# Kernel tuning notes

Measured on AMD Instinct MI355X. Metric: run time of the kernel, lower is better.

## Reference

```python
import jax, jax.numpy as jnp
import numpy as np

RADIUS = 0.4
NSAMPLE = 32
NORMALIZE_DP = True


def setup_inputs() -> dict:
    key = jax.random.key(0)
    k1, k2, k3 = jax.random.split(key, 3)
    B, N, K, C = 2, 16384, 4096, 128
    xyz = jax.random.normal(k1, (B, N, 3), dtype=jnp.float32)
    new_xyz = jax.random.normal(k2, (B, K, 3), dtype=jnp.float32)
    features = jax.random.normal(k3, (B, C, N), dtype=jnp.float32)
    return {"xyz": xyz, "new_xyz": new_xyz, "features": features}


def _ball_query(radius, nsample, xyz, new_xyz):
    # xyz: (B,N,3), new_xyz: (B,K,3) -> indices (B,K,nsample) int32
    N = xyz.shape[1]
    # squared distances via ||a||^2 + ||b||^2 - 2 a.b  -> (B,K,N)
    d2 = (jnp.sum(new_xyz * new_xyz, -1)[:, :, None]
          + jnp.sum(xyz * xyz, -1)[:, None, :]
          - 2.0 * jnp.einsum('bkd,bnd->bkn', new_xyz, xyz))
    mask = d2 < radius * radius
    # key = point index if inside ball else N (sentinel); take nsample smallest
    key = jnp.where(mask, jnp.arange(N, dtype=jnp.int32), jnp.int32(N))
    neg_top, _ = jax.lax.top_k(-key, nsample)  # (B,K,nsample)
    idx = -neg_top
    # pointnet2 semantics: pad with first in-radius index (0 if ball empty)
    first = idx[..., :1]
    first = jnp.where(first < N, first, 0)
    idx = jnp.where(idx < N, idx, first)
    return idx


def _group(features, idx):
    # features: (B,C,N), idx: (B,K,ns) -> (B,C,K,ns)
    return jax.vmap(lambda f, i: f[:, i])(features, idx)


def reference(xyz, new_xyz, features):
    idx = _ball_query(RADIUS, NSAMPLE, xyz, new_xyz)          # (B,K,ns)
    xyz_t = jnp.transpose(xyz, (0, 2, 1))                      # (B,3,N)
    grouped_xyz = _group(xyz_t, idx)                           # (B,3,K,ns)
    grouped_xyz = grouped_xyz - jnp.transpose(new_xyz, (0, 2, 1))[..., None]
    if NORMALIZE_DP:
        grouped_xyz = grouped_xyz / RADIUS
    grouped_features = _group(features, idx)                   # (B,C,K,ns)
    return (grouped_xyz, grouped_features)
```

## Files before the change

### kernel.cpp

```cpp
#include <hip/hip_runtime.h>

#define BB 2
#define NN 16384
#define KK 4096
#define CC 128
#define SS 32
#define BKK (BB * KK)

typedef float vfloat4 __attribute__((ext_vector_type(4)));

__global__ __launch_bounds__(1024) void prep_sort_kernel(
    const float* __restrict__ xyz, const float* __restrict__ new_xyz,
    float* __restrict__ xyzw, int* __restrict__ qmap)
{
    const int t = threadIdx.x;

    if (blockIdx.x == 0) {
        __shared__ int hist[64];
        __shared__ int base[64];
        __shared__ unsigned char bk[BKK];

        if (t < 64) hist[t] = 0;
        __syncthreads();

#pragma unroll
        for (int c = 0; c < BKK / 1024; ++c) {
            const int q = c * 1024 + t;
            const float* p = new_xyz + (size_t)q * 3;
            const float qq = p[0] * p[0] + p[1] * p[1] + p[2] * p[2];
            int bkt = (int)(qq * 8.0f);
            bkt = bkt > 63 ? 63 : bkt;
            bk[q] = (unsigned char)bkt;
            atomicAdd(&hist[bkt], 1);
        }
        __syncthreads();

        if (t == 0) {
            int s = 0;
#pragma unroll
            for (int i = 0; i < 64; ++i) { base[i] = s; s += hist[i]; }
        }
        __syncthreads();

#pragma unroll
        for (int c = 0; c < BKK / 1024; ++c) {
            const int q = c * 1024 + t;
            const int pos = atomicAdd(&base[bk[q]], 1);
            qmap[pos] = q;
        }
    } else {
        const int i = (blockIdx.x - 1) * 1024 + t;
        const float* p = xyz + (size_t)i * 3;
        const float x = p[0], y = p[1], z = p[2];
        const float pp = __fadd_rn(__fadd_rn(__fmul_rn(x, x), __fmul_rn(y, y)),
                                   __fmul_rn(z, z));
        vfloat4 v = {x, y, z, pp};
        *(vfloat4*)(xyzw + (size_t)i * 4) = v;
    }
}

__global__ __launch_bounds__(256) void ball_transpose_kernel(
    const float* __restrict__ xyzw,
    const float* __restrict__ new_xyz,
    const int* __restrict__ qmap,
    const float* __restrict__ feat,
    int* __restrict__ idx_buf,
    float* __restrict__ feat_t)
{
    __shared__ float tile[32][133];

    const int t = threadIdx.x;

    if (blockIdx.x < BKK / 4) {
        const int wave = t >> 6;
        const int lane = t & 63;
        const int qi   = qmap[blockIdx.x * 4 + wave];
        const int b    = qi >> 12;
        const int k    = qi & (KK - 1);

        const float R2 = (float)(0.4 * 0.4);

        const float* q = new_xyz + (size_t)(b * KK + k) * 3;
        const float qx = q[0], qy = q[1], qz = q[2];
        const float qq = __fadd_rn(__fadd_rn(__fmul_rn(qx, qx), __fmul_rn(qy, qy)),
                                   __fmul_rn(qz, qz));

        const vfloat4* xw = (const vfloat4*)xyzw + (size_t)b * NN;
        int* out = idx_buf + (size_t)qi * SS;

        int cnt = 0;
        int first = -1;

        auto process = [&](int base, vfloat4 v) {
            const float dot = __fadd_rn(__fadd_rn(__fmul_rn(qx, v.x), __fmul_rn(qy, v.y)),
                                        __fmul_rn(qz, v.z));
            const float d2 = __fsub_rn(__fadd_rn(qq, v.w), __fmul_rn(2.0f, dot));
            const bool inball = d2 < R2;
            const unsigned long long mask = __ballot(inball);
            if (mask) {
                if (first < 0) first = base + (int)__builtin_ctzll(mask);
                if (inball) {
                    const int pos = cnt + __popcll(mask & ((1ull << lane) - 1ull));
                    if (pos < SS) out[pos] = base + lane;
                }
                cnt += __popcll(mask);
            }
        };

        vfloat4 v0 = xw[lane];
        vfloat4 v1 = xw[64 + lane];
        vfloat4 v2 = xw[128 + lane];
        vfloat4 v3 = xw[192 + lane];

        for (int base = 0; base < NN; base += 256) {
            const int nb = (base + 256 < NN) ? base + 256 : 0;
            vfloat4 u0 = xw[nb + lane];
            vfloat4 u1 = xw[nb + 64 + lane];
            vfloat4 u2 = xw[nb + 128 + lane];
            vfloat4 u3 = xw[nb + 192 + lane];

            process(base, v0);
            process(base + 64, v1);
            process(base + 128, v2);
            process(base + 192, v3);
            if (cnt >= SS) break;

            v0 = u0; v1 = u1; v2 = u2; v3 = u3;
        }

        const int fill = (first < 0) ? 0 : first;
        if (lane < SS && lane >= cnt) out[lane] = fill;
    } else {
        const int tb = blockIdx.x - BKK / 4;
        const int b  = tb >> 9;
        const int n0 = (tb & 511) * 32;

#pragma unroll
        for (int i = 0; i < 4; ++i) {
            const int li = i * 256 + t;
            const int c  = li >> 3;
            const int n4 = (li & 7) * 4;
            const vfloat4 v = *(const vfloat4*)(feat + ((size_t)b * CC + c) * NN + n0 + n4);
            tile[n4 + 0][c] = v.x;
            tile[n4 + 1][c] = v.y;
            tile[n4 + 2][c] = v.z;
            tile[n4 + 3][c] = v.w;
        }
        __syncthreads();

#pragma unroll
        for (int i = 0; i < 4; ++i) {
            const int li = i * 256 + t;
            const int n  = li >> 5;
            const int c4 = (li & 31) * 4;
            vfloat4 v;
            v.x = tile[n][c4 + 0];
            v.y = tile[n][c4 + 1];
            v.z = tile[n][c4 + 2];
            v.w = tile[n][c4 + 3];
            *(vfloat4*)(feat_t + ((size_t)(b * NN + n0 + n)) * CC + c4) = v;
        }
    }
}

__global__ __launch_bounds__(256) void group_kernel(
    const float* __restrict__ xyzw,
    const float* __restrict__ new_xyz,
    const float* __restrict__ feat_t,
    const int*   __restrict__ idx_buf,
    float* __restrict__ out)
{
    __shared__ float tile[SS * CC];
    __shared__ float txyz[3][SS];

    const int t    = threadIdx.x;
    const int l    = t & 63;
    const int w    = t >> 6;
    const int bk   = blockIdx.x;
    const int b    = bk >> 12;
    const int k    = bk & (KK - 1);
    const int half = l >> 5;
    const int cl   = l & 31;

#pragma unroll
    for (int p = 0; p < 4; ++p) {
        const int r = 8 * w + 2 * p;
        const int s = r + half;
        const int n = idx_buf[bk * SS + s];
        const int chunk = cl ^ ((s >> 2) & 7);
        const float* src = feat_t + ((size_t)(b * NN + n)) * CC + 4 * chunk;
        __builtin_amdgcn_global_load_lds(
            (const __attribute__((address_space(1))) void*)src,
            (__attribute__((address_space(3))) void*)(tile + r * CC),
            16, 0, 0);
    }

    if (t < SS) {
        const int n = idx_buf[bk * SS + t];
        const float* q = new_xyz + (size_t)bk * 3;
        const vfloat4 wv = *((const vfloat4*)xyzw + (size_t)b * NN + n);
        txyz[0][t] = (wv.x - q[0]) / 0.4f;
        txyz[1][t] = (wv.y - q[1]) / 0.4f;
        txyz[2][t] = (wv.z - q[2]) / 0.4f;
    }

    __syncthreads();

    float* out_xyz  = out;
    float* out_feat = out + (size_t)BB * 3 * KK * SS;

    const int sq = t & 7;
    const int c0 = t >> 3;
#pragma unroll
    for (int p = 0; p < 4; ++p) {
        const int c  = c0 + 32 * p;
        const int co = (((c >> 2) ^ sq) << 2) + (c & 3);
        vfloat4 v;
        v.x = tile[(4 * sq + 0) * CC + co];
        v.y = tile[(4 * sq + 1) * CC + co];
        v.z = tile[(4 * sq + 2) * CC + co];
        v.w = tile[(4 * sq + 3) * CC + co];
        __builtin_nontemporal_store(
            v, (vfloat4*)(out_feat + (((size_t)(b * CC + c) * KK + k) * SS + 4 * sq)));
    }

    if (t < 24) {
        const int d   = t >> 3;
        const int sq2 = t & 7;
        const vfloat4 v = *(vfloat4*)&txyz[d][4 * sq2];
        __builtin_nontemporal_store(
            v, (vfloat4*)(out_xyz + (((size_t)(b * 3 + d) * KK + k) * SS + 4 * sq2)));
    }
}

extern "C" void kernel_launch(void* const* d_in, const int* in_sizes, int n_in,
                              void* d_out, int out_size, void* d_ws, size_t ws_size,
                              hipStream_t stream) {
    const float* xyz     = (const float*)d_in[0];
    const float* new_xyz = (const float*)d_in[1];
    const float* feat    = (const float*)d_in[2];
    float* out = (float*)d_out;

    int*   idx_buf = (int*)d_ws;
    float* xyzw    = (float*)((char*)d_ws + (1 << 20));
    float* feat_t  = (float*)((char*)d_ws + (1 << 20) + (512 << 10));
    int*   qmap    = (int*)((char*)d_ws + (1 << 20) + (512 << 10) + (CC * NN * BB) * 4);

    prep_sort_kernel<<<dim3(33), dim3(1024), 0, stream>>>(
        xyz, new_xyz, xyzw, qmap);

    ball_transpose_kernel<<<dim3(BKK / 4 + BB * (NN / 32)), dim3(256), 0, stream>>>(
        xyzw, new_xyz, qmap, feat, idx_buf, feat_t);

    group_kernel<<<dim3(BKK), dim3(256), 0, stream>>>(
        xyzw, new_xyz, feat_t, idx_buf, out);
}
```

Before: 82.67 us.

## Double-buffer two queries per group block and halve ball-query block size

```diff
diff --git a/kernel.cpp b/kernel.cpp
--- a/kernel.cpp
+++ b/kernel.cpp
@@ -59,7 +59,7 @@
     }
 }
 
-__global__ __launch_bounds__(256) void ball_transpose_kernel(
+__global__ __launch_bounds__(128) void ball_transpose_kernel(
     const float* __restrict__ xyzw,
     const float* __restrict__ new_xyz,
     const int* __restrict__ qmap,
@@ -71,10 +71,10 @@
 
     const int t = threadIdx.x;
 
-    if (blockIdx.x < BKK / 4) {
+    if (blockIdx.x < BKK / 2) {
         const int wave = t >> 6;
         const int lane = t & 63;
-        const int qi   = qmap[blockIdx.x * 4 + wave];
+        const int qi   = qmap[blockIdx.x * 2 + wave];
         const int b    = qi >> 12;
         const int k    = qi & (KK - 1);
 
@@ -131,13 +131,13 @@
         const int fill = (first < 0) ? 0 : first;
         if (lane < SS && lane >= cnt) out[lane] = fill;
     } else {
-        const int tb = blockIdx.x - BKK / 4;
+        const int tb = blockIdx.x - BKK / 2;
         const int b  = tb >> 9;
         const int n0 = (tb & 511) * 32;
 
 #pragma unroll
-        for (int i = 0; i < 4; ++i) {
-            const int li = i * 256 + t;
+        for (int i = 0; i < 8; ++i) {
+            const int li = i * 128 + t;
             const int c  = li >> 3;
             const int n4 = (li & 7) * 4;
             const vfloat4 v = *(const vfloat4*)(feat + ((size_t)b * CC + c) * NN + n0 + n4);
@@ -149,8 +149,8 @@
         __syncthreads();
 
 #pragma unroll
-        for (int i = 0; i < 4; ++i) {
-            const int li = i * 256 + t;
+        for (int i = 0; i < 8; ++i) {
+            const int li = i * 128 + t;
             const int n  = li >> 5;
             const int c4 = (li & 31) * 4;
             vfloat4 v;
@@ -170,66 +170,124 @@
     const int*   __restrict__ idx_buf,
     float* __restrict__ out)
 {
-    __shared__ float tile[SS * CC];
-    __shared__ float txyz[3][SS];
+    __shared__ float tileA[SS * CC];
+    __shared__ float tileB[SS * CC];
+    __shared__ float txyzA[3][SS];
+    __shared__ float txyzB[3][SS];
 
     const int t    = threadIdx.x;
     const int l    = t & 63;
     const int w    = t >> 6;
-    const int bk   = blockIdx.x;
-    const int b    = bk >> 12;
-    const int k    = bk & (KK - 1);
+    const int bk0  = blockIdx.x * 2;
+    const int bk1  = bk0 + 1;
     const int half = l >> 5;
     const int cl   = l & 31;
 
-#pragma unroll
-    for (int p = 0; p < 4; ++p) {
-        const int r = 8 * w + 2 * p;
-        const int s = r + half;
-        const int n = idx_buf[bk * SS + s];
-        const int chunk = cl ^ ((s >> 2) & 7);
-        const float* src = feat_t + ((size_t)(b * NN + n)) * CC + 4 * chunk;
-        __builtin_amdgcn_global_load_lds(
-            (const __attribute__((address_space(1))) void*)src,
-            (__attribute__((address_space(3))) void*)(tile + r * CC),
-            16, 0, 0);
-    }
-
-    if (t < SS) {
-        const int n = idx_buf[bk * SS + t];
-        const float* q = new_xyz + (size_t)bk * 3;
-        const vfloat4 wv = *((const vfloat4*)xyzw + (size_t)b * NN + n);
-        txyz[0][t] = (wv.x - q[0]) / 0.4f;
-        txyz[1][t] = (wv.y - q[1]) / 0.4f;
-        txyz[2][t] = (wv.z - q[2]) / 0.4f;
-    }
-
-    __syncthreads();
-
     float* out_xyz  = out;
     float* out_feat = out + (size_t)BB * 3 * KK * SS;
 
-    const int sq = t & 7;
-    const int c0 = t >> 3;
-#pragma unroll
-    for (int p = 0; p < 4; ++p) {
-        const int c  = c0 + 32 * p;
-        const int co = (((c >> 2) ^ sq) << 2) + (c & 3);
-        vfloat4 v;
-        v.x = tile[(4 * sq + 0) * CC + co];
-        v.y = tile[(4 * sq + 1) * CC + co];
-        v.z = tile[(4 * sq + 2) * CC + co];
-        v.w = tile[(4 * sq + 3) * CC + co];
-        __builtin_nontemporal_store(
-            v, (vfloat4*)(out_feat + (((size_t)(b * CC + c) * KK + k) * SS + 4 * sq)));
-    }
-
-    if (t < 24) {
-        const int d   = t >> 3;
-        const int sq2 = t & 7;
-        const vfloat4 v = *(vfloat4*)&txyz[d][4 * sq2];
-        __builtin_nontemporal_store(
-            v, (vfloat4*)(out_xyz + (((size_t)(b * 3 + d) * KK + k) * SS + 4 * sq2)));
+    {
+        const int b = bk0 >> 12;
+#pragma unroll
+        for (int p = 0; p < 4; ++p) {
+            const int r = 8 * w + 2 * p;
+            const int s = r + half;
+            const int n = idx_buf[bk0 * SS + s];
+            const int chunk = cl ^ ((s >> 2) & 7);
+            const float* src = feat_t + ((size_t)(b * NN + n)) * CC + 4 * chunk;
+            __builtin_amdgcn_global_load_lds(
+                (const __attribute__((address_space(1))) void*)src,
+                (__attribute__((address_space(3))) void*)(tileA + r * CC),
+                16, 0, 0);
+        }
+        if (t < SS) {
+            const int n = idx_buf[bk0 * SS + t];
+            const float* q = new_xyz + (size_t)bk0 * 3;
+            const vfloat4 wv = *((const vfloat4*)xyzw + (size_t)b * NN + n);
+            txyzA[0][t] = (wv.x - q[0]) / 0.4f;
+            txyzA[1][t] = (wv.y - q[1]) / 0.4f;
+            txyzA[2][t] = (wv.z - q[2]) / 0.4f;
+        }
+    }
+
+    __syncthreads();
+
+    {
+        const int b = bk1 >> 12;
+#pragma unroll
+        for (int p = 0; p < 4; ++p) {
+            const int r = 8 * w + 2 * p;
+            const int s = r + half;
+            const int n = idx_buf[bk1 * SS + s];
+            const int chunk = cl ^ ((s >> 2) & 7);
+            const float* src = feat_t + ((size_t)(b * NN + n)) * CC + 4 * chunk;
+            __builtin_amdgcn_global_load_lds(
+                (const __attribute__((address_space(1))) void*)src,
+                (__attribute__((address_space(3))) void*)(tileB + r * CC),
+                16, 0, 0);
+        }
+        if (t < SS) {
+            const int n = idx_buf[bk1 * SS + t];
+            const float* q = new_xyz + (size_t)bk1 * 3;
+            const vfloat4 wv = *((const vfloat4*)xyzw + (size_t)b * NN + n);
+            txyzB[0][t] = (wv.x - q[0]) / 0.4f;
+            txyzB[1][t] = (wv.y - q[1]) / 0.4f;
+            txyzB[2][t] = (wv.z - q[2]) / 0.4f;
+        }
+    }
+
+    {
+        const int b  = bk0 >> 12;
+        const int k  = bk0 & (KK - 1);
+        const int sq = t & 7;
+        const int c0 = t >> 3;
+#pragma unroll
+        for (int p = 0; p < 4; ++p) {
+            const int c  = c0 + 32 * p;
+            const int co = (((c >> 2) ^ sq) << 2) + (c & 3);
+            vfloat4 v;
+            v.x = tileA[(4 * sq + 0) * CC + co];
+            v.y = tileA[(4 * sq + 1) * CC + co];
+            v.z = tileA[(4 * sq + 2) * CC + co];
+            v.w = tileA[(4 * sq + 3) * CC + co];
+            __builtin_nontemporal_store(
+                v, (vfloat4*)(out_feat + (((size_t)(b * CC + c) * KK + k) * SS + 4 * sq)));
+        }
+        if (t < 24) {
+            const int d   = t >> 3;
+            const int sq2 = t & 7;
+            const vfloat4 v = *(vfloat4*)&txyzA[d][4 * sq2];
+            __builtin_nontemporal_store(
+                v, (vfloat4*)(out_xyz + (((size_t)(b * 3 + d) * KK + k) * SS + 4 * sq2)));
+        }
+    }
+
+    __syncthreads();
+
+    {
+        const int b  = bk1 >> 12;
+        const int k  = bk1 & (KK - 1);
+        const int sq = t & 7;
+        const int c0 = t >> 3;
+#pragma unroll
+        for (int p = 0; p < 4; ++p) {
+            const int c  = c0 + 32 * p;
+            const int co = (((c >> 2) ^ sq) << 2) + (c & 3);
+            vfloat4 v;
+            v.x = tileB[(4 * sq + 0) * CC + co];
+            v.y = tileB[(4 * sq + 1) * CC + co];
+            v.z = tileB[(4 * sq + 2) * CC + co];
+            v.w = tileB[(4 * sq + 3) * CC + co];
+            __builtin_nontemporal_store(
+                v, (vfloat4*)(out_feat + (((size_t)(b * CC + c) * KK + k) * SS + 4 * sq)));
+        }
+        if (t < 24) {
+            const int d   = t >> 3;
+            const int sq2 = t & 7;
+            const vfloat4 v = *(vfloat4*)&txyzB[d][4 * sq2];
+            __builtin_nontemporal_store(
+                v, (vfloat4*)(out_xyz + (((size_t)(b * 3 + d) * KK + k) * SS + 4 * sq2)));
+        }
     }
 }
 
@@ -249,9 +307,9 @@
     prep_sort_kernel<<<dim3(33), dim3(1024), 0, stream>>>(
         xyz, new_xyz, xyzw, qmap);
 
-    ball_transpose_kernel<<<dim3(BKK / 4 + BB * (NN / 32)), dim3(256), 0, stream>>>(
+    ball_transpose_kernel<<<dim3(BKK / 2 + BB * (NN / 32)), dim3(128), 0, stream>>>(
         xyzw, new_xyz, qmap, feat, idx_buf, feat_t);
 
-    group_kernel<<<dim3(BKK), dim3(256), 0, stream>>>(
+    group_kernel<<<dim3(BKK / 2), dim3(256), 0, stream>>>(
         xyzw, new_xyz, feat_t, idx_buf, out);
 }
```

New measurement: 84.34 us. +2.0%, slower.
